# Performance work log

Measured on AMD Instinct MI355X. Metric: run time of the kernel, lower is better.

Reference implementation:

```python
import jax, jax.numpy as jnp
import numpy as np

TWO_PI = 2.0 * np.pi
EPS = 1e-6

# mixture packed layout along last axis (7): [weight, px, py, cxx, cxy, cyx, cyy]

def unpack(m):
    w = m[..., 0]
    p = m[..., 1:3]
    C = m[..., 3:7].reshape(m.shape[:-1] + (2, 2))
    return w, p, C

def pack(w, p, C):
    return jnp.concatenate([w[..., None], p, C.reshape(C.shape[:-2] + (4,))], axis=-1)

def det2(C):
    return C[..., 0, 0] * C[..., 1, 1] - C[..., 0, 1] * C[..., 1, 0]

def inv2(C):
    d = det2(C)[..., None, None]
    adj = jnp.stack([
        jnp.stack([C[..., 1, 1], -C[..., 0, 1]], axis=-1),
        jnp.stack([-C[..., 1, 0], C[..., 0, 0]], axis=-1)], axis=-2)
    return adj / d

def component_integrals(w, C):
    # integral of an amplitude-parameterized 2D gaussian: w * 2*pi * sqrt(det C)
    return w * TWO_PI * jnp.sqrt(jnp.maximum(det2(C), EPS))

def gm_convolve(data, kernel):
    # data [B,Li,Nd,7], kernel [Lo,Li,Nk,7] -> [B,Lo,Li*Nd*Nk,7]
    wd, pd, Cd = unpack(data)
    wk, pk, Ck = unpack(kernel)
    dd = det2(Cd)[:, None, :, :, None]              # [B,1,Li,Nd,1]
    dk = det2(Ck)[None, :, :, None, :]              # [1,Lo,Li,1,Nk]
    Cs = Cd[:, None, :, :, None, :, :] + Ck[None, :, :, None, :, :, :]  # [B,Lo,Li,Nd,Nk,2,2]
    ps = pd[:, None, :, :, None, :] + pk[None, :, :, None, :, :]        # [B,Lo,Li,Nd,Nk,2]
    # amplitude of convolved gaussian so that integrals multiply
    ws = (wd[:, None, :, :, None] * wk[None, :, :, None, :]
          * TWO_PI * jnp.sqrt(dd * dk / jnp.maximum(det2(Cs), EPS)))
    m = pack(ws, ps, Cs)
    B, Lo = m.shape[0], m.shape[1]
    return m.reshape(B, Lo, -1, 7)

def eval_at_centers(w, p, C):
    # value of the whole mixture at each component center; [.., N]
    Ci = inv2(C)                                        # [..,N,2,2]
    diff = p[..., :, None, :] - p[..., None, :, :]      # [..,K,N,2]
    md = jnp.einsum('...kni,...nij,...knj->...kn', diff, Ci, diff)
    return jnp.einsum('...n,...kn->...k', w, jnp.exp(-0.5 * md))

def relu_fit(m, bias, n_out):
    # fitting-based ReLU: rescale each component so the mixture matches
    # relu(m(x)+b) at the centers, then keep the n_out largest components
    w, p, C = unpack(m)
    v = eval_at_centers(w, p, C) + bias[None, :, None]  # [B,L,N]
    scale = jax.nn.relu(v) / (jnp.abs(v) + EPS)
    w2 = w * scale
    _, idx = jax.lax.top_k(jnp.abs(w2), n_out)          # [B,L,n_out]
    w_s = jnp.take_along_axis(w2, idx, axis=-1)
    p_s = jnp.take_along_axis(p, jnp.broadcast_to(idx[..., None], idx.shape + (2,)), axis=-2)
    Cf = C.reshape(C.shape[:-2] + (4,))
    C_s = jnp.take_along_axis(Cf, jnp.broadcast_to(idx[..., None], idx.shape + (4,)), axis=-2)
    return pack(w_s, p_s, C_s.reshape(C_s.shape[:-1] + (2, 2)))

def batchnorm(m, per_gaussian):
    w, p, C = unpack(m)
    tot = jnp.sum(jnp.abs(component_integrals(w, C)), axis=-1, keepdims=True)  # [B,L,1]
    if not per_gaussian:
        tot = jnp.mean(tot, axis=0, keepdims=True)      # batch statistic per channel
    return pack(w / (tot + EPS), p, C)

def integrate(m):
    w, _, C = unpack(m)
    return jnp.sum(component_integrals(w, C), axis=-1)  # [B,L]

def forward(in_x, kernel1, kernel2, kernel3, bias1, bias2, bias3):
    x = batchnorm(in_x, per_gaussian=True)   # bn0
    x = gm_convolve(x, kernel1)              # [B,5,320,7]
    x = relu_fit(x, bias1, 25)
    x = batchnorm(x, per_gaussian=False)
    x = gm_convolve(x, kernel2)              # [B,6,625,7]
    x = relu_fit(x, bias2, 12)
    x = batchnorm(x, per_gaussian=False)
    x = gm_convolve(x, kernel3)              # [B,10,360,7]
    x = relu_fit(x, bias3, 5)
    x = batchnorm(x, per_gaussian=False)
    out = jax.nn.log_softmax(integrate(x), axis=1)
    return out.reshape(-1, 10)

def _make_kernel(key, lo, li, nk, weight_sd, position_range, covariance_range):
    kw, kp = jax.random.split(key)
    w = jax.random.normal(kw, (lo, li, nk)) * weight_sd
    p = jax.random.uniform(kp, (lo, li, nk, 2), minval=-position_range, maxval=position_range)
    C = jnp.broadcast_to(covariance_range * jnp.eye(2), (lo, li, nk, 2, 2))
    return pack(w, p, C).astype(jnp.float32)

def setup_inputs() -> dict:
    key = jax.random.key(0)
    k = jax.random.split(key, 8)
    B, NIN, NK = 32, 64, 5
    w = jax.random.uniform(k[0], (B, 1, NIN), minval=0.05, maxval=1.0)
    p = jax.random.uniform(k[1], (B, 1, NIN, 2), minval=-14.0, maxval=14.0)
    cdiag = jax.random.uniform(k[2], (B, 1, NIN, 2), minval=0.5, maxval=2.0)
    C = jnp.zeros((B, 1, NIN, 2, 2)).at[..., 0, 0].set(cdiag[..., 0]).at[..., 1, 1].set(cdiag[..., 1])
    in_x = pack(w, p, C).astype(jnp.float32)
    return {
        'in_x': in_x,
        'kernel1': _make_kernel(k[3], 5, 1, NK, 0.4, 2.0, 0.5),
        'kernel2': _make_kernel(k[4], 6, 5, NK, 0.04, 4.0, 2.0),
        'kernel3': _make_kernel(k[5], 10, 6, NK, 0.025, 8.0, 4.0),
        'bias1': jnp.zeros((5,), jnp.float32),
        'bias2': jnp.zeros((6,), jnp.float32),
        'bias3': jnp.zeros((10,), jnp.float32),
    }

def reference(in_x, kernel1, kernel2, kernel3, bias1, bias2, bias3):
    return forward(in_x, kernel1, kernel2, kernel3, bias1, bias2, bias3)
```

## Files before the change

### kernel.cpp

```cpp
#include <hip/hip_runtime.h>

#define TWO_PI_F 6.283185307179586f
#define EPS_F 1e-6f
#define LOG2E_F 1.4426950408889634f
#define BATCH 32

#if __has_builtin(__builtin_amdgcn_exp2f)
#define EXP2F(x) __builtin_amdgcn_exp2f(x)
#else
#define EXP2F(x) exp2f(x)
#endif

typedef float v2f __attribute__((ext_vector_type(2)));

__device__ __forceinline__ float sane(float x) {
    return ((__float_as_uint(x) & 0x7f800000u) == 0x7f800000u) ? 0.f : x;
}

template<int LO, int LI, int ND, int NK, int NCOMP, int KOUT,
         int KP, int KUSE, int TPG, int G, bool FIRST>
__global__ __launch_bounds__(TPG*G) void layer_kernel(
    const float* __restrict__ in_x,
    const float* __restrict__ prev_sel,
    const float* __restrict__ prev_tot,
    const float* __restrict__ kern,
    const float* __restrict__ bias,
    float* __restrict__ out_sel,
    float* __restrict__ out_tot)
{
    static_assert(KP*KUSE >= NCOMP, "k-dim must cover NCOMP");
    static_assert(KUSE <= TPG, "k lanes within group");
    constexpr int KDIM   = KP*KUSE;
    constexpr int NT     = TPG * G;
    constexpr int CHUNK  = (NCOMP + G - 1) / G;
    constexpr int NPADT  = G*CHUNK + 4;
    constexpr int NCOMP4 = (NCOMP + 3) & ~3;
    constexpr int NQn    = NCOMP4 / 4;
    constexpr int NPAIR  = KP / 2;
    constexpr int PPAD   = NPAIR > 0 ? NPAIR : 1;
    constexpr bool ODD   = (KP & 1) != 0;
    constexpr int CPOS_SZ = (KDIM > NCOMP) ? KDIM : NCOMP;

    const int b   = blockIdx.x / LO;
    const int lo  = blockIdx.x % LO;
    const int tid = threadIdx.x;
    const int g   = tid / TPG;
    const int kt  = tid % TPG;
    const bool active = (kt < KUSE);

    struct StageT {
        float4 d_c[LI*ND];
        float4 k_c[LI*NK];
        float  d_w[LI*ND], d_px[LI*ND], d_py[LI*ND];
        float  k_w[LI*NK], k_px[LI*NK], k_py[LI*NK];
    };
    constexpr size_t ACCB = (size_t)G*TPG*KP * sizeof(float);
    constexpr size_t UB   = sizeof(StageT) > ACCB ? sizeof(StageT) : ACCB;
    __shared__ __align__(16) unsigned char u_smem[UB];
    StageT& st    = *reinterpret_cast<StageT*>(u_smem);
    float* accbuf = reinterpret_cast<float*>(u_smem);

    __shared__ float2 cPos[CPOS_SZ];
    __shared__ float4 nP[NPADT];
    __shared__ float4 nQ[NPADT];
    __shared__ float4 cC[NCOMP];
    __shared__ float  w2s[NCOMP];
    __shared__ __align__(16) float a2s[NCOMP4];
    __shared__ __align__(16) float scr[64];
    __shared__ float  selint[32];
    __shared__ float  dscale[LI];
    __shared__ float  ptot[FIRST ? 1 : BATCH*LI];

    if constexpr (FIRST) {
        if (tid < ND) {
            const float* s = in_x + (size_t)(b*ND + tid)*7;
            const float w  = sane(s[0]);
            const float c0 = sane(s[3]), c1 = sane(s[4]), c2 = sane(s[5]), c3 = sane(s[6]);
            st.d_w[tid] = w; st.d_px[tid] = sane(s[1]); st.d_py[tid] = sane(s[2]);
            st.d_c[tid] = make_float4(c0, c1, c2, c3);
            const float det = c0*c3 - c1*c2;
            scr[tid] = sane(fabsf(w) * TWO_PI_F * sqrtf(fmaxf(det, EPS_F)));
        }
        __syncthreads();
        if (tid == 0) {
            float s = 0.f;
            const float4* s4 = (const float4*)scr;
            for (int i = 0; i < 16; ++i) {
                const float4 v = s4[i];
                s += v.x; s += v.y; s += v.z; s += v.w;
            }
            dscale[0] = 1.f / (s + EPS_F);
        }
        __syncthreads();
        if (tid < ND) st.d_w[tid] = sane(st.d_w[tid] * dscale[0]);
    } else {
        for (int i = tid; i < BATCH*LI; i += NT) ptot[i] = prev_tot[i];
        __syncthreads();
        if (tid < LI) {
            float s = 0.f;
            #pragma unroll 1
            for (int bb = 0; bb < BATCH; ++bb) s += ptot[bb*LI + tid];
            dscale[tid] = 1.f / (s / (float)BATCH + EPS_F);
        }
        __syncthreads();
        if (tid < LI*ND) {
            const int li = tid / ND;
            const float* s = prev_sel + (size_t)(b*LI*ND + tid)*7;
            st.d_w[tid]  = sane(s[0] * dscale[li]);
            st.d_px[tid] = s[1]; st.d_py[tid] = s[2];
            st.d_c[tid]  = make_float4(s[3], s[4], s[5], s[6]);
        }
    }
    if (tid < LI*NK) {
        const float* s = kern + (size_t)(lo*LI*NK + tid)*7;
        st.k_w[tid]  = sane(s[0]);
        st.k_px[tid] = sane(s[1]); st.k_py[tid] = sane(s[2]);
        st.k_c[tid]  = make_float4(sane(s[3]), sane(s[4]), sane(s[5]), sane(s[6]));
    }
    __syncthreads();

    for (int i = tid; i < NCOMP; i += NT) {
        const int li = i / (ND*NK);
        const int r  = i % (ND*NK);
        const int nd = r / NK, nk = r % NK;
        const int di = li*ND + nd, ki = li*NK + nk;
        const float4 dc = st.d_c[di], kc = st.k_c[ki];
        const float c0 = dc.x + kc.x, c1 = dc.y + kc.y, c2 = dc.z + kc.z, c3 = dc.w + kc.w;
        const float dd = dc.x*dc.w - dc.y*dc.z;
        const float dk = kc.x*kc.w - kc.y*kc.z;
        const float ds = c0*c3 - c1*c2;
        const float w  = sane(st.d_w[di]*st.k_w[ki]*TWO_PI_F*sqrtf(fmaxf(dd*dk, 0.f) / fmaxf(ds, EPS_F)));
        const float px = sane(st.d_px[di] + st.k_px[ki]);
        const float py = sane(st.d_py[di] + st.k_py[ki]);
        const float inv = -0.5f * LOG2E_F / ds;
        const float a   = sane(c3*inv);
        const float bb  = sane(-(c1 + c2)*inv);
        const float cc  = sane(c0*inv);
        const float dd2 = sane(-(2.f*a*px + bb*py));
        const float ee  = sane(-(2.f*cc*py + bb*px));
        const float ff  = sane((a*px + bb*py)*px + cc*py*py);
        cPos[i] = make_float2(px, py);
        nP[i]   = make_float4(a, bb, cc, dd2);
        nQ[i]   = make_float4(ee, ff, w, 0.f);
        cC[i]   = make_float4(sane(c0), sane(c1), sane(c2), sane(c3));
    }
    for (int i = NCOMP + tid; i < NPADT; i += NT) {
        nP[i] = make_float4(0.f, 0.f, 0.f, 0.f);
        nQ[i] = make_float4(0.f, 0.f, 0.f, 0.f);
    }
    for (int i = NCOMP + tid; i < CPOS_SZ; i += NT) cPos[i] = make_float2(0.f, 0.f);
    __syncthreads();

    v2f kxP[PPAD], kyP[PPAD], kx2P[PPAD], ky2P[PPAD], kxyP[PPAD], accP[PPAD];
    float kxS = 0.f, kyS = 0.f, kx2S = 0.f, ky2S = 0.f, kxyS = 0.f, accS = 0.f;
    #pragma unroll
    for (int p = 0; p < NPAIR; ++p) {
        float x0 = 0.f, y0 = 0.f, x1 = 0.f, y1 = 0.f;
        if (active) {
            const float2 p0 = cPos[kt + (2*p    )*KUSE];
            const float2 p1 = cPos[kt + (2*p + 1)*KUSE];
            x0 = p0.x; y0 = p0.y; x1 = p1.x; y1 = p1.y;
        }
        v2f kx; kx.x = x0; kx.y = x1;
        v2f ky; ky.x = y0; ky.y = y1;
        kxP[p] = kx; kyP[p] = ky;
        kx2P[p] = kx*kx; ky2P[p] = ky*ky; kxyP[p] = kx*ky;
        v2f z; z.x = 0.f; z.y = 0.f; accP[p] = z;
    }
    if constexpr (ODD) {
        if (active) { const float2 pz = cPos[kt + (KP-1)*KUSE]; kxS = pz.x; kyS = pz.y; }
        kx2S = kxS*kxS; ky2S = kyS*kyS; kxyS = kxS*kyS;
    }
    {
        const int n0 = g*CHUNK;
        const float4* __restrict__ bP = &nP[n0];
        const float4* __restrict__ bQ = &nQ[n0];
        float4 P0 = bP[0], Q0 = bQ[0];
        float4 P1 = bP[1], Q1 = bQ[1];
        float4 P2 = bP[2], Q2 = bQ[2];
        float4 P3 = bP[3], Q3 = bQ[3];
        int nr = 4;

#define PHB_STEP(PP,QQ)                                                       \
        {   const float4 Pn_ = bP[nr], Qn_ = bQ[nr]; ++nr;                    \
            v2f Pa; Pa.x = PP.x; Pa.y = PP.x;                                 \
            v2f Pb; Pb.x = PP.y; Pb.y = PP.y;                                 \
            v2f Pc; Pc.x = PP.z; Pc.y = PP.z;                                 \
            v2f Pd; Pd.x = PP.w; Pd.y = PP.w;                                 \
            v2f Qe; Qe.x = QQ.x; Qe.y = QQ.x;                                 \
            v2f Qf; Qf.x = QQ.y; Qf.y = QQ.y;                                 \
            v2f Qw; Qw.x = QQ.z; Qw.y = QQ.z;                                 \
            _Pragma("unroll")                                                 \
            for (int p = 0; p < NPAIR; ++p) {                                 \
                const v2f md = __builtin_elementwise_fma(Pa, kx2P[p],         \
                               __builtin_elementwise_fma(Pb, kxyP[p],         \
                               __builtin_elementwise_fma(Pc, ky2P[p],         \
                               __builtin_elementwise_fma(Pd, kxP[p],          \
                               __builtin_elementwise_fma(Qe, kyP[p], Qf)))));  \
                v2f ex; ex.x = EXP2F(md.x); ex.y = EXP2F(md.y);               \
                accP[p] = __builtin_elementwise_fma(Qw, ex, accP[p]);         \
            }                                                                 \
            if constexpr (ODD) {                                              \
                const float md = fmaf(PP.x, kx2S,                             \
                                 fmaf(PP.y, kxyS,                             \
                                 fmaf(PP.z, ky2S,                             \
                                 fmaf(PP.w, kxS,                              \
                                 fmaf(QQ.x, kyS, QQ.y)))));                   \
                accS = fmaf(QQ.z, EXP2F(md), accS);                           \
            }                                                                 \
            PP = Pn_; QQ = Qn_; }

        #pragma unroll 1
        for (int i4 = 0; i4 < CHUNK/4; ++i4) {
            PHB_STEP(P0, Q0)
            PHB_STEP(P1, Q1)
            PHB_STEP(P2, Q2)
            PHB_STEP(P3, Q3)
        }
        if constexpr ((CHUNK % 4) >= 1) PHB_STEP(P0, Q0)
        if constexpr ((CHUNK % 4) >= 2) PHB_STEP(P1, Q1)
        if constexpr ((CHUNK % 4) >= 3) PHB_STEP(P2, Q2)
#undef PHB_STEP
    }
    float acc[KP];
    #pragma unroll
    for (int p = 0; p < NPAIR; ++p) { acc[2*p] = accP[p].x; acc[2*p+1] = accP[p].y; }
    if constexpr (ODD) acc[KP-1] = accS;

    if (active) {
        #pragma unroll
        for (int j = 0; j < KP; ++j) accbuf[(g*TPG + kt)*KP + j] = acc[j];
    }
    __syncthreads();

    const float bi = bias[lo];
    for (int k = tid; k < NCOMP; k += NT) {
        const int j2  = k / KUSE;
        const int kt2 = k - j2*KUSE;
        float s = accbuf[kt2*KP + j2];
        #pragma unroll 1
        for (int g2 = 1; g2 < G; ++g2) s += accbuf[(g2*TPG + kt2)*KP + j2];
        const float v  = s + bi;
        const float sc = fmaxf(v, 0.f) / (fabsf(v) + EPS_F);
        const float ww = sane(nQ[k].z * sc);
        w2s[k] = ww;
        a2s[k] = fabsf(ww);
    }
    for (int i = NCOMP + tid; i < NCOMP4; i += NT) a2s[i] = -1.f;
    __syncthreads();

    constexpr int CQ = (NQn + G - 1) / G;
    int rank[KP];
    float myv[KP];
    #pragma unroll
    for (int j = 0; j < KP; ++j) { rank[j] = 0; myv[j] = -2.f; }
    if (active) {
        #pragma unroll
        for (int j = 0; j < KP; ++j) {
            if (kt + j*KUSE < NCOMP) myv[j] = a2s[kt + j*KUSE];
        }
        const int q0 = g*CQ;
        const int q1 = (q0 + CQ < NQn) ? (q0 + CQ) : NQn;
        #pragma unroll 1
        for (int q = q0; q < q1; ++q) {
            const float4 v4 = ((const float4*)a2s)[q];
            #pragma unroll
            for (int c = 0; c < 4; ++c) {
                const float vj = (c == 0) ? v4.x : (c == 1) ? v4.y : (c == 2) ? v4.z : v4.w;
                const int   jj = 4*q + c;
                #pragma unroll
                for (int j = 0; j < KP; ++j) {
                    const int myk = kt + j*KUSE;
                    rank[j] += (vj > myv[j] || (vj == myv[j] && jj < myk)) ? 1 : 0;
                }
            }
        }
        #pragma unroll
        for (int j = 0; j < KP; ++j) accbuf[(g*TPG + kt)*KP + j] = (float)rank[j];
    }
    __syncthreads();

    for (int k = tid; k < NCOMP; k += NT) {
        const int j2  = k / KUSE;
        const int kt2 = k - j2*KUSE;
        int r = 0;
        #pragma unroll 1
        for (int g2 = 0; g2 < G; ++g2) r += (int)accbuf[(g2*TPG + kt2)*KP + j2];
        if (r < KOUT) {
            const float2 p = cPos[k];
            const float4 c = cC[k];
            const float ww = w2s[k];
            float* dst = out_sel + (size_t)((b*LO + lo)*KOUT + r)*7;
            dst[0] = ww; dst[1] = p.x; dst[2] = p.y;
            dst[3] = c.x; dst[4] = c.y; dst[5] = c.z; dst[6] = c.w;
            const float det = c.x*c.w - c.y*c.z;
            selint[r] = sane(fabsf(ww) * TWO_PI_F * sqrtf(fmaxf(det, EPS_F)));
        }
    }
    __syncthreads();
    if (tid == 0) {
        float s = 0.f;
        #pragma unroll 1
        for (int i = 0; i < KOUT; ++i) s += selint[i];
        out_tot[b*LO + lo] = s;
    }
}

__global__ __launch_bounds__(64) void final_kernel(
    const float* __restrict__ sel3,
    const float* __restrict__ tot3,
    float* __restrict__ out)
{
    const int b = blockIdx.x;
    const int tid = threadIdx.x;
    __shared__ float scale3[10], integ[10], red2[2];
    if (tid < 10) {
        float s = 0.f;
        for (int bb = 0; bb < BATCH; ++bb) s += tot3[bb*10 + tid];
        scale3[tid] = 1.f / (s / (float)BATCH + EPS_F);
    }
    __syncthreads();
    if (tid < 10) {
        float s = 0.f;
        const float* base = sel3 + (size_t)((b*10 + tid)*5)*7;
        for (int kk = 0; kk < 5; ++kk) {
            const float* c = base + kk*7;
            const float det = c[3]*c[6] - c[4]*c[5];
            s += c[0] * scale3[tid] * TWO_PI_F * sqrtf(fmaxf(det, EPS_F));
        }
        integ[tid] = sane(s);
    }
    __syncthreads();
    if (tid == 0) {
        float m = -1e30f;
        for (int l = 0; l < 10; ++l) m = fmaxf(m, integ[l]);
        float ss = 0.f;
        for (int l = 0; l < 10; ++l) ss += __expf(integ[l] - m);
        red2[0] = m; red2[1] = logf(ss);
    }
    __syncthreads();
    if (tid < 10) out[b*10 + tid] = integ[tid] - red2[0] - red2[1];
}

extern "C" void kernel_launch(void* const* d_in, const int* in_sizes, int n_in,
                              void* d_out, int out_size, void* d_ws, size_t ws_size,
                              hipStream_t stream)
{
    const float* in_x = (const float*)d_in[0];
    const float* k1   = (const float*)d_in[1];
    const float* k2   = (const float*)d_in[2];
    const float* k3   = (const float*)d_in[3];
    const float* b1   = (const float*)d_in[4];
    const float* b2   = (const float*)d_in[5];
    const float* b3   = (const float*)d_in[6];
    float* out = (float*)d_out;

    float* ws = (float*)d_ws;
    float* sel1 = ws;
    float* tot1 = ws + 28000;
    float* sel2 = ws + 28160;
    float* tot2 = ws + 44288;
    float* sel3 = ws + 44480;
    float* tot3 = ws + 55680;

    layer_kernel<5, 1, 64, 5, 320, 25, 5, 64, 64, 16, true>
        <<<BATCH*5, 1024, 0, stream>>>(in_x, nullptr, nullptr, k1, b1, sel1, tot1);
    layer_kernel<6, 5, 25, 5, 625, 12, 10, 64, 64, 8, false>
        <<<BATCH*6, 512, 0, stream>>>(nullptr, sel1, tot1, k2, b2, sel2, tot2);
    layer_kernel<10, 6, 12, 5, 360, 5, 6, 60, 64, 12, false>
        <<<BATCH*10, 768, 0, stream>>>(nullptr, sel2, tot2, k3, b3, sel3, tot3);
    final_kernel<<<BATCH, 64, 0, stream>>>(sel3, tot3, out);
}
```

Before: 163.3 us.

## Fuse all layers into one cooperative persistent kernel with grid syncs

Replaces the four separate kernel launches with a single cooperative kernel of 256 blocks of 1024 threads that runs the three layers and the final reduction, separated by grid-wide syncs. Layer 3's 320 units are spread over 256 blocks, so 64 blocks process two units. Layer 2 is retiled (KP 10 to 5, TPG 128, 1024 threads) to fit the uniform block size, and threads outside the groups sit idle. The goal is to remove launch gaps and inter-kernel drain, at the cost of grid-sync overhead, idle threads in some layers, and a serialized second pass for layer 3.

Result: slower. 236.1 us (+44.6%).

```diff
diff --git a/kernel.cpp b/kernel.cpp
--- a/kernel.cpp
+++ b/kernel.cpp
@@ -1,4 +1,7 @@
 #include <hip/hip_runtime.h>
+#include <hip/hip_cooperative_groups.h>
+
+namespace cg = cooperative_groups;
 
 #define TWO_PI_F 6.283185307179586f
 #define EPS_F 1e-6f
@@ -17,9 +20,35 @@
     return ((__float_as_uint(x) & 0x7f800000u) == 0x7f800000u) ? 0.f : x;
 }
 
+
+template<int LI, int ND, int NK, int NCOMP, int KP, int TPG, int G, bool FIRST>
+struct LayerSmem {
+    static constexpr int CHUNK  = (NCOMP + G - 1) / G;
+    static constexpr int NPADT  = G*CHUNK + 4;
+    static constexpr int NCOMP4 = (NCOMP + 3) & ~3;
+    struct StageT {
+        float4 d_c[LI*ND];
+        float4 k_c[LI*NK];
+        float  d_w[LI*ND], d_px[LI*ND], d_py[LI*ND];
+        float  k_w[LI*NK], k_px[LI*NK], k_py[LI*NK];
+    };
+    union U { StageT st; float accbuf[G*TPG*KP]; } u;
+    float2 cPos[NCOMP];
+    float4 nP[NPADT];
+    float4 nQ[NPADT];
+    float4 cC[NCOMP];
+    float  w2s[NCOMP];
+    alignas(16) float a2s[NCOMP4];
+    alignas(16) float scr[64];
+    float selint[32];
+    float dscale[LI];
+    float ptot[FIRST ? 4 : BATCH*LI];
+};
+
 template<int LO, int LI, int ND, int NK, int NCOMP, int KOUT,
-         int KP, int KUSE, int TPG, int G, bool FIRST>
-__global__ __launch_bounds__(TPG*G) void layer_kernel(
+         int KP, int TPG, int G, bool FIRST, int NTB>
+__device__ void layer_body(
+    unsigned char* smem_raw, const int unit, const int tid,
     const float* __restrict__ in_x,
     const float* __restrict__ prev_sel,
     const float* __restrict__ prev_tot,
@@ -28,48 +57,27 @@
     float* __restrict__ out_sel,
     float* __restrict__ out_tot)
 {
-    static_assert(KP*KUSE >= NCOMP, "k-dim must cover NCOMP");
-    static_assert(KUSE <= TPG, "k lanes within group");
-    constexpr int KDIM   = KP*KUSE;
-    constexpr int NT     = TPG * G;
+    constexpr int KUSE   = NCOMP / KP;
+    static_assert(KUSE * KP == NCOMP, "exact k tiling required");
     constexpr int CHUNK  = (NCOMP + G - 1) / G;
-    constexpr int NPADT  = G*CHUNK + 4;
     constexpr int NCOMP4 = (NCOMP + 3) & ~3;
     constexpr int NQn    = NCOMP4 / 4;
     constexpr int NPAIR  = KP / 2;
     constexpr int PPAD   = NPAIR > 0 ? NPAIR : 1;
     constexpr bool ODD   = (KP & 1) != 0;
-    constexpr int CPOS_SZ = (KDIM > NCOMP) ? KDIM : NCOMP;
-
-    const int b   = blockIdx.x / LO;
-    const int lo  = blockIdx.x % LO;
-    const int tid = threadIdx.x;
+    using SM = LayerSmem<LI, ND, NK, NCOMP, KP, TPG, G, FIRST>;
+    constexpr int NPADT  = SM::NPADT;
+
+    SM& S = *reinterpret_cast<SM*>(smem_raw);
+    float* accbuf = S.u.accbuf;
+    auto&  st     = S.u.st;
+
+    const int b   = unit / LO;
+    const int lo  = unit % LO;
     const int g   = tid / TPG;
     const int kt  = tid % TPG;
-    const bool active = (kt < KUSE);
-
-    struct StageT {
-        float4 d_c[LI*ND];
-        float4 k_c[LI*NK];
-        float  d_w[LI*ND], d_px[LI*ND], d_py[LI*ND];
-        float  k_w[LI*NK], k_px[LI*NK], k_py[LI*NK];
-    };
-    constexpr size_t ACCB = (size_t)G*TPG*KP * sizeof(float);
-    constexpr size_t UB   = sizeof(StageT) > ACCB ? sizeof(StageT) : ACCB;
-    __shared__ __align__(16) unsigned char u_smem[UB];
-    StageT& st    = *reinterpret_cast<StageT*>(u_smem);
-    float* accbuf = reinterpret_cast<float*>(u_smem);
-
-    __shared__ float2 cPos[CPOS_SZ];
-    __shared__ float4 nP[NPADT];
-    __shared__ float4 nQ[NPADT];
-    __shared__ float4 cC[NCOMP];
-    __shared__ float  w2s[NCOMP];
-    __shared__ __align__(16) float a2s[NCOMP4];
-    __shared__ __align__(16) float scr[64];
-    __shared__ float  selint[32];
-    __shared__ float  dscale[LI];
-    __shared__ float  ptot[FIRST ? 1 : BATCH*LI];
+    const bool ingrp  = (g < G);
+    const bool active = ingrp && (kt < KUSE);
 
     if constexpr (FIRST) {
         if (tid < ND) {
@@ -79,34 +87,34 @@
             st.d_w[tid] = w; st.d_px[tid] = sane(s[1]); st.d_py[tid] = sane(s[2]);
             st.d_c[tid] = make_float4(c0, c1, c2, c3);
             const float det = c0*c3 - c1*c2;
-            scr[tid] = sane(fabsf(w) * TWO_PI_F * sqrtf(fmaxf(det, EPS_F)));
+            S.scr[tid] = sane(fabsf(w) * TWO_PI_F * sqrtf(fmaxf(det, EPS_F)));
         }
         __syncthreads();
         if (tid == 0) {
             float s = 0.f;
-            const float4* s4 = (const float4*)scr;
+            const float4* s4 = (const float4*)S.scr;
             for (int i = 0; i < 16; ++i) {
                 const float4 v = s4[i];
                 s += v.x; s += v.y; s += v.z; s += v.w;
             }
-            dscale[0] = 1.f / (s + EPS_F);
-        }
-        __syncthreads();
-        if (tid < ND) st.d_w[tid] = sane(st.d_w[tid] * dscale[0]);
+            S.dscale[0] = 1.f / (s + EPS_F);
+        }
+        __syncthreads();
+        if (tid < ND) st.d_w[tid] = sane(st.d_w[tid] * S.dscale[0]);
     } else {
-        for (int i = tid; i < BATCH*LI; i += NT) ptot[i] = prev_tot[i];
+        for (int i = tid; i < BATCH*LI; i += NTB) S.ptot[i] = prev_tot[i];
         __syncthreads();
         if (tid < LI) {
             float s = 0.f;
             #pragma unroll 1
-            for (int bb = 0; bb < BATCH; ++bb) s += ptot[bb*LI + tid];
-            dscale[tid] = 1.f / (s / (float)BATCH + EPS_F);
+            for (int bb = 0; bb < BATCH; ++bb) s += S.ptot[bb*LI + tid];
+            S.dscale[tid] = 1.f / (s / (float)BATCH + EPS_F);
         }
         __syncthreads();
         if (tid < LI*ND) {
             const int li = tid / ND;
             const float* s = prev_sel + (size_t)(b*LI*ND + tid)*7;
-            st.d_w[tid]  = sane(s[0] * dscale[li]);
+            st.d_w[tid]  = sane(s[0] * S.dscale[li]);
             st.d_px[tid] = s[1]; st.d_py[tid] = s[2];
             st.d_c[tid]  = make_float4(s[3], s[4], s[5], s[6]);
         }
@@ -119,7 +127,7 @@
     }
     __syncthreads();
 
-    for (int i = tid; i < NCOMP; i += NT) {
+    for (int i = tid; i < NCOMP; i += NTB) {
         const int li = i / (ND*NK);
         const int r  = i % (ND*NK);
         const int nd = r / NK, nk = r % NK;
@@ -139,93 +147,96 @@
         const float dd2 = sane(-(2.f*a*px + bb*py));
         const float ee  = sane(-(2.f*cc*py + bb*px));
         const float ff  = sane((a*px + bb*py)*px + cc*py*py);
-        cPos[i] = make_float2(px, py);
-        nP[i]   = make_float4(a, bb, cc, dd2);
-        nQ[i]   = make_float4(ee, ff, w, 0.f);
-        cC[i]   = make_float4(sane(c0), sane(c1), sane(c2), sane(c3));
-    }
-    for (int i = NCOMP + tid; i < NPADT; i += NT) {
-        nP[i] = make_float4(0.f, 0.f, 0.f, 0.f);
-        nQ[i] = make_float4(0.f, 0.f, 0.f, 0.f);
-    }
-    for (int i = NCOMP + tid; i < CPOS_SZ; i += NT) cPos[i] = make_float2(0.f, 0.f);
-    __syncthreads();
-
-    v2f kxP[PPAD], kyP[PPAD], kx2P[PPAD], ky2P[PPAD], kxyP[PPAD], accP[PPAD];
-    float kxS = 0.f, kyS = 0.f, kx2S = 0.f, ky2S = 0.f, kxyS = 0.f, accS = 0.f;
-    #pragma unroll
-    for (int p = 0; p < NPAIR; ++p) {
-        float x0 = 0.f, y0 = 0.f, x1 = 0.f, y1 = 0.f;
-        if (active) {
-            const float2 p0 = cPos[kt + (2*p    )*KUSE];
-            const float2 p1 = cPos[kt + (2*p + 1)*KUSE];
-            x0 = p0.x; y0 = p0.y; x1 = p1.x; y1 = p1.y;
-        }
-        v2f kx; kx.x = x0; kx.y = x1;
-        v2f ky; ky.x = y0; ky.y = y1;
-        kxP[p] = kx; kyP[p] = ky;
-        kx2P[p] = kx*kx; ky2P[p] = ky*ky; kxyP[p] = kx*ky;
-        v2f z; z.x = 0.f; z.y = 0.f; accP[p] = z;
-    }
-    if constexpr (ODD) {
-        if (active) { const float2 pz = cPos[kt + (KP-1)*KUSE]; kxS = pz.x; kyS = pz.y; }
-        kx2S = kxS*kxS; ky2S = kyS*kyS; kxyS = kxS*kyS;
-    }
-    {
-        const int n0 = g*CHUNK;
-        const float4* __restrict__ bP = &nP[n0];
-        const float4* __restrict__ bQ = &nQ[n0];
-        float4 P0 = bP[0], Q0 = bQ[0];
-        float4 P1 = bP[1], Q1 = bQ[1];
-        float4 P2 = bP[2], Q2 = bQ[2];
-        float4 P3 = bP[3], Q3 = bQ[3];
-        int nr = 4;
-
-#define PHB_STEP(PP,QQ)                                                       \
-        {   const float4 Pn_ = bP[nr], Qn_ = bQ[nr]; ++nr;                    \
-            v2f Pa; Pa.x = PP.x; Pa.y = PP.x;                                 \
-            v2f Pb; Pb.x = PP.y; Pb.y = PP.y;                                 \
-            v2f Pc; Pc.x = PP.z; Pc.y = PP.z;                                 \
-            v2f Pd; Pd.x = PP.w; Pd.y = PP.w;                                 \
-            v2f Qe; Qe.x = QQ.x; Qe.y = QQ.x;                                 \
-            v2f Qf; Qf.x = QQ.y; Qf.y = QQ.y;                                 \
-            v2f Qw; Qw.x = QQ.z; Qw.y = QQ.z;                                 \
-            _Pragma("unroll")                                                 \
-            for (int p = 0; p < NPAIR; ++p) {                                 \
-                const v2f md = __builtin_elementwise_fma(Pa, kx2P[p],         \
-                               __builtin_elementwise_fma(Pb, kxyP[p],         \
-                               __builtin_elementwise_fma(Pc, ky2P[p],         \
-                               __builtin_elementwise_fma(Pd, kxP[p],          \
-                               __builtin_elementwise_fma(Qe, kyP[p], Qf)))));  \
-                v2f ex; ex.x = EXP2F(md.x); ex.y = EXP2F(md.y);               \
-                accP[p] = __builtin_elementwise_fma(Qw, ex, accP[p]);         \
-            }                                                                 \
-            if constexpr (ODD) {                                              \
-                const float md = fmaf(PP.x, kx2S,                             \
-                                 fmaf(PP.y, kxyS,                             \
-                                 fmaf(PP.z, ky2S,                             \
-                                 fmaf(PP.w, kxS,                              \
-                                 fmaf(QQ.x, kyS, QQ.y)))));                   \
-                accS = fmaf(QQ.z, EXP2F(md), accS);                           \
-            }                                                                 \
-            PP = Pn_; QQ = Qn_; }
-
-        #pragma unroll 1
-        for (int i4 = 0; i4 < CHUNK/4; ++i4) {
-            PHB_STEP(P0, Q0)
-            PHB_STEP(P1, Q1)
-            PHB_STEP(P2, Q2)
-            PHB_STEP(P3, Q3)
-        }
-        if constexpr ((CHUNK % 4) >= 1) PHB_STEP(P0, Q0)
-        if constexpr ((CHUNK % 4) >= 2) PHB_STEP(P1, Q1)
-        if constexpr ((CHUNK % 4) >= 3) PHB_STEP(P2, Q2)
-#undef PHB_STEP
-    }
+        S.cPos[i] = make_float2(px, py);
+        S.nP[i]   = make_float4(a, bb, cc, dd2);
+        S.nQ[i]   = make_float4(ee, ff, w, 0.f);
+        S.cC[i]   = make_float4(sane(c0), sane(c1), sane(c2), sane(c3));
+    }
+    for (int i = NCOMP + tid; i < NPADT; i += NTB) {
+        S.nP[i] = make_float4(0.f, 0.f, 0.f, 0.f);
+        S.nQ[i] = make_float4(0.f, 0.f, 0.f, 0.f);
+    }
+    __syncthreads();
+
     float acc[KP];
     #pragma unroll
-    for (int p = 0; p < NPAIR; ++p) { acc[2*p] = accP[p].x; acc[2*p+1] = accP[p].y; }
-    if constexpr (ODD) acc[KP-1] = accS;
+    for (int j = 0; j < KP; ++j) acc[j] = 0.f;
+    if (ingrp) {
+        v2f kxP[PPAD], kyP[PPAD], kx2P[PPAD], ky2P[PPAD], kxyP[PPAD], accP[PPAD];
+        float kxS = 0.f, kyS = 0.f, kx2S = 0.f, ky2S = 0.f, kxyS = 0.f, accS = 0.f;
+        #pragma unroll
+        for (int p = 0; p < NPAIR; ++p) {
+            float x0 = 0.f, y0 = 0.f, x1 = 0.f, y1 = 0.f;
+            if (active) {
+                const float2 p0 = S.cPos[kt + (2*p    )*KUSE];
+                const float2 p1 = S.cPos[kt + (2*p + 1)*KUSE];
+                x0 = p0.x; y0 = p0.y; x1 = p1.x; y1 = p1.y;
+            }
+            v2f kx; kx.x = x0; kx.y = x1;
+            v2f ky; ky.x = y0; ky.y = y1;
+            kxP[p] = kx; kyP[p] = ky;
+            kx2P[p] = kx*kx; ky2P[p] = ky*ky; kxyP[p] = kx*ky;
+            v2f z; z.x = 0.f; z.y = 0.f; accP[p] = z;
+        }
+        if constexpr (ODD) {
+            if (active) { const float2 pz = S.cPos[kt + (KP-1)*KUSE]; kxS = pz.x; kyS = pz.y; }
+            kx2S = kxS*kxS; ky2S = kyS*kyS; kxyS = kxS*kyS;
+        }
+        {
+            const int n0 = g*CHUNK;
+            const float4* __restrict__ bP = &S.nP[n0];
+            const float4* __restrict__ bQ = &S.nQ[n0];
+            float4 P0 = bP[0], Q0 = bQ[0];
+            float4 P1 = bP[1], Q1 = bQ[1];
+            float4 P2 = bP[2], Q2 = bQ[2];
+            float4 P3 = bP[3], Q3 = bQ[3];
+            int nr = 4;
+
+#define PHB_STEP(PP,QQ)                                                       \
+            {   const float4 Pn_ = bP[nr], Qn_ = bQ[nr]; ++nr;                \
+                v2f Pa; Pa.x = PP.x; Pa.y = PP.x;                             \
+                v2f Pb; Pb.x = PP.y; Pb.y = PP.y;                             \
+                v2f Pc; Pc.x = PP.z; Pc.y = PP.z;                             \
+                v2f Pd; Pd.x = PP.w; Pd.y = PP.w;                             \
+                v2f Qe; Qe.x = QQ.x; Qe.y = QQ.x;                             \
+                v2f Qf; Qf.x = QQ.y; Qf.y = QQ.y;                             \
+                v2f Qw; Qw.x = QQ.z; Qw.y = QQ.z;                             \
+                _Pragma("unroll")                                             \
+                for (int p = 0; p < NPAIR; ++p) {                             \
+                    const v2f md = __builtin_elementwise_fma(Pa, kx2P[p],     \
+                                   __builtin_elementwise_fma(Pb, kxyP[p],     \
+                                   __builtin_elementwise_fma(Pc, ky2P[p],     \
+                                   __builtin_elementwise_fma(Pd, kxP[p],      \
+                                   __builtin_elementwise_fma(Qe, kyP[p], Qf)))));  \
+                    v2f ex; ex.x = EXP2F(md.x); ex.y = EXP2F(md.y);           \
+                    accP[p] = __builtin_elementwise_fma(Qw, ex, accP[p]);     \
+                }                                                             \
+                if constexpr (ODD) {                                          \
+                    const float md = fmaf(PP.x, kx2S,                         \
+                                     fmaf(PP.y, kxyS,                         \
+                                     fmaf(PP.z, ky2S,                         \
+                                     fmaf(PP.w, kxS,                          \
+                                     fmaf(QQ.x, kyS, QQ.y)))));               \
+                    accS = fmaf(QQ.z, EXP2F(md), accS);                       \
+                }                                                             \
+                PP = Pn_; QQ = Qn_; }
+
+            #pragma unroll 1
+            for (int i4 = 0; i4 < CHUNK/4; ++i4) {
+                PHB_STEP(P0, Q0)
+                PHB_STEP(P1, Q1)
+                PHB_STEP(P2, Q2)
+                PHB_STEP(P3, Q3)
+            }
+            if constexpr ((CHUNK % 4) >= 1) PHB_STEP(P0, Q0)
+            if constexpr ((CHUNK % 4) >= 2) PHB_STEP(P1, Q1)
+            if constexpr ((CHUNK % 4) >= 3) PHB_STEP(P2, Q2)
+#undef PHB_STEP
+        }
+        #pragma unroll
+        for (int p = 0; p < NPAIR; ++p) { acc[2*p] = accP[p].x; acc[2*p+1] = accP[p].y; }
+        if constexpr (ODD) acc[KP-1] = accS;
+    }
 
     if (active) {
         #pragma unroll
@@ -234,36 +245,34 @@
     __syncthreads();
 
     const float bi = bias[lo];
-    for (int k = tid; k < NCOMP; k += NT) {
+    for (int k = tid; k < NCOMP; k += NTB) {
+        const int kt2 = k % KUSE;
         const int j2  = k / KUSE;
-        const int kt2 = k - j2*KUSE;
         float s = accbuf[kt2*KP + j2];
         #pragma unroll 1
         for (int g2 = 1; g2 < G; ++g2) s += accbuf[(g2*TPG + kt2)*KP + j2];
         const float v  = s + bi;
         const float sc = fmaxf(v, 0.f) / (fabsf(v) + EPS_F);
-        const float ww = sane(nQ[k].z * sc);
-        w2s[k] = ww;
-        a2s[k] = fabsf(ww);
-    }
-    for (int i = NCOMP + tid; i < NCOMP4; i += NT) a2s[i] = -1.f;
+        const float ww = sane(S.nQ[k].z * sc);
+        S.w2s[k] = ww;
+        S.a2s[k] = fabsf(ww);
+    }
+    for (int i = NCOMP + tid; i < NCOMP4; i += NTB) S.a2s[i] = -1.f;
     __syncthreads();
 
     constexpr int CQ = (NQn + G - 1) / G;
     int rank[KP];
     float myv[KP];
     #pragma unroll
-    for (int j = 0; j < KP; ++j) { rank[j] = 0; myv[j] = -2.f; }
+    for (int j = 0; j < KP; ++j) rank[j] = 0;
     if (active) {
         #pragma unroll
-        for (int j = 0; j < KP; ++j) {
-            if (kt + j*KUSE < NCOMP) myv[j] = a2s[kt + j*KUSE];
-        }
+        for (int j = 0; j < KP; ++j) myv[j] = S.a2s[kt + j*KUSE];
         const int q0 = g*CQ;
         const int q1 = (q0 + CQ < NQn) ? (q0 + CQ) : NQn;
         #pragma unroll 1
         for (int q = q0; q < q1; ++q) {
-            const float4 v4 = ((const float4*)a2s)[q];
+            const float4 v4 = ((const float4*)S.a2s)[q];
             #pragma unroll
             for (int c = 0; c < 4; ++c) {
                 const float vj = (c == 0) ? v4.x : (c == 1) ? v4.y : (c == 2) ? v4.z : v4.w;
@@ -280,66 +289,104 @@
     }
     __syncthreads();
 
-    for (int k = tid; k < NCOMP; k += NT) {
+    for (int k = tid; k < NCOMP; k += NTB) {
+        const int kt2 = k % KUSE;
         const int j2  = k / KUSE;
-        const int kt2 = k - j2*KUSE;
         int r = 0;
         #pragma unroll 1
         for (int g2 = 0; g2 < G; ++g2) r += (int)accbuf[(g2*TPG + kt2)*KP + j2];
         if (r < KOUT) {
-            const float2 p = cPos[k];
-            const float4 c = cC[k];
-            const float ww = w2s[k];
-            float* dst = out_sel + (size_t)((b*LO + lo)*KOUT + r)*7;
+            const float2 p = S.cPos[k];
+            const float4 c = S.cC[k];
+            const float ww = S.w2s[k];
+            float* dst = out_sel + (size_t)(unit*KOUT + r)*7;
             dst[0] = ww; dst[1] = p.x; dst[2] = p.y;
             dst[3] = c.x; dst[4] = c.y; dst[5] = c.z; dst[6] = c.w;
             const float det = c.x*c.w - c.y*c.z;
-            selint[r] = sane(fabsf(ww) * TWO_PI_F * sqrtf(fmaxf(det, EPS_F)));
+            S.selint[r] = sane(fabsf(ww) * TWO_PI_F * sqrtf(fmaxf(det, EPS_F)));
         }
     }
     __syncthreads();
     if (tid == 0) {
         float s = 0.f;
         #pragma unroll 1
-        for (int i = 0; i < KOUT; ++i) s += selint[i];
-        out_tot[b*LO + lo] = s;
-    }
+        for (int i = 0; i < KOUT; ++i) s += S.selint[i];
+        out_tot[unit] = s;
+    }
+    __syncthreads();
 }
 
-__global__ __launch_bounds__(64) void final_kernel(
-    const float* __restrict__ sel3,
-    const float* __restrict__ tot3,
+struct FinalSmem { float scale3[10]; float integ[10]; float red2[2]; };
+
+constexpr size_t S1B = sizeof(LayerSmem<1, 64, 5, 320, 5, 64, 16, true>);
+constexpr size_t S2B = sizeof(LayerSmem<5, 25, 5, 625, 5, 128, 8, false>);
+constexpr size_t S3B = sizeof(LayerSmem<6, 12, 5, 360, 6, 64, 12, false>);
+constexpr size_t SMEM_BYTES =
+    (S1B > S2B ? (S1B > S3B ? S1B : S3B) : (S2B > S3B ? S2B : S3B));
+
+__global__ __launch_bounds__(1024) void mega_kernel(
+    const float* __restrict__ in_x,
+    const float* __restrict__ k1, const float* __restrict__ k2,
+    const float* __restrict__ k3,
+    const float* __restrict__ b1, const float* __restrict__ b2,
+    const float* __restrict__ b3,
+    float* __restrict__ sel1, float* __restrict__ tot1,
+    float* __restrict__ sel2, float* __restrict__ tot2,
+    float* __restrict__ sel3, float* __restrict__ tot3,
     float* __restrict__ out)
 {
-    const int b = blockIdx.x;
+    __shared__ __align__(16) unsigned char smem[SMEM_BYTES];
+    cg::grid_group grid = cg::this_grid();
+    const int blk = blockIdx.x;
     const int tid = threadIdx.x;
-    __shared__ float scale3[10], integ[10], red2[2];
-    if (tid < 10) {
-        float s = 0.f;
-        for (int bb = 0; bb < BATCH; ++bb) s += tot3[bb*10 + tid];
-        scale3[tid] = 1.f / (s / (float)BATCH + EPS_F);
-    }
-    __syncthreads();
-    if (tid < 10) {
-        float s = 0.f;
-        const float* base = sel3 + (size_t)((b*10 + tid)*5)*7;
-        for (int kk = 0; kk < 5; ++kk) {
-            const float* c = base + kk*7;
-            const float det = c[3]*c[6] - c[4]*c[5];
-            s += c[0] * scale3[tid] * TWO_PI_F * sqrtf(fmaxf(det, EPS_F));
-        }
-        integ[tid] = sane(s);
-    }
-    __syncthreads();
-    if (tid == 0) {
-        float m = -1e30f;
-        for (int l = 0; l < 10; ++l) m = fmaxf(m, integ[l]);
-        float ss = 0.f;
-        for (int l = 0; l < 10; ++l) ss += __expf(integ[l] - m);
-        red2[0] = m; red2[1] = logf(ss);
-    }
-    __syncthreads();
-    if (tid < 10) out[b*10 + tid] = integ[tid] - red2[0] - red2[1];
+
+    if (blk < BATCH*5)
+        layer_body<5, 1, 64, 5, 320, 25, 5, 64, 16, true, 1024>(
+            smem, blk, tid, in_x, nullptr, nullptr, k1, b1, sel1, tot1);
+    grid.sync();
+
+    if (blk < BATCH*6)
+        layer_body<6, 5, 25, 5, 625, 12, 5, 128, 8, false, 1024>(
+            smem, blk, tid, nullptr, sel1, tot1, k2, b2, sel2, tot2);
+    grid.sync();
+
+    layer_body<10, 6, 12, 5, 360, 5, 6, 64, 12, false, 1024>(
+        smem, blk, tid, nullptr, sel2, tot2, k3, b3, sel3, tot3);
+    if (blk < BATCH*10 - 256)
+        layer_body<10, 6, 12, 5, 360, 5, 6, 64, 12, false, 1024>(
+            smem, blk + 256, tid, nullptr, sel2, tot2, k3, b3, sel3, tot3);
+    grid.sync();
+
+    if (blk < BATCH) {
+        FinalSmem& FS = *reinterpret_cast<FinalSmem*>(smem);
+        const int b = blk;
+        if (tid < 10) {
+            float s = 0.f;
+            for (int bb = 0; bb < BATCH; ++bb) s += tot3[bb*10 + tid];
+            FS.scale3[tid] = 1.f / (s / (float)BATCH + EPS_F);
+        }
+        __syncthreads();
+        if (tid < 10) {
+            float s = 0.f;
+            const float* base = sel3 + (size_t)((b*10 + tid)*5)*7;
+            for (int kk = 0; kk < 5; ++kk) {
+                const float* c = base + kk*7;
+                const float det = c[3]*c[6] - c[4]*c[5];
+                s += c[0] * FS.scale3[tid] * TWO_PI_F * sqrtf(fmaxf(det, EPS_F));
+            }
+            FS.integ[tid] = sane(s);
+        }
+        __syncthreads();
+        if (tid == 0) {
+            float m = -1e30f;
+            for (int l = 0; l < 10; ++l) m = fmaxf(m, FS.integ[l]);
+            float ss = 0.f;
+            for (int l = 0; l < 10; ++l) ss += __expf(FS.integ[l] - m);
+            FS.red2[0] = m; FS.red2[1] = logf(ss);
+        }
+        __syncthreads();
+        if (tid < 10) out[b*10 + tid] = FS.integ[tid] - FS.red2[0] - FS.red2[1];
+    }
 }
 
 extern "C" void kernel_launch(void* const* d_in, const int* in_sizes, int n_in,
@@ -363,11 +410,12 @@
     float* sel3 = ws + 44480;
     float* tot3 = ws + 55680;
 
-    layer_kernel<5, 1, 64, 5, 320, 25, 5, 64, 64, 16, true>
-        <<<BATCH*5, 1024, 0, stream>>>(in_x, nullptr, nullptr, k1, b1, sel1, tot1);
-    layer_kernel<6, 5, 25, 5, 625, 12, 10, 64, 64, 8, false>
-        <<<BATCH*6, 512, 0, stream>>>(nullptr, sel1, tot1, k2, b2, sel2, tot2);
-    layer_kernel<10, 6, 12, 5, 360, 5, 6, 60, 64, 12, false>
-        <<<BATCH*10, 768, 0, stream>>>(nullptr, sel2, tot2, k3, b3, sel3, tot3);
-    final_kernel<<<BATCH, 64, 0, stream>>>(sel3, tot3, out);
+    void* args[] = {
+        (void*)&in_x, (void*)&k1, (void*)&k2, (void*)&k3,
+        (void*)&b1, (void*)&b2, (void*)&b3,
+        (void*)&sel1, (void*)&tot1, (void*)&sel2, (void*)&tot2,
+        (void*)&sel3, (void*)&tot3, (void*)&out
+    };
+    hipLaunchCooperativeKernel((const void*)mega_kernel,
+                               dim3(256), dim3(1024), args, 0, stream);
 }
```
